# Kernel optimization log

Hardware: AMD Instinct MI355X
Metric: run time of the kernel (lower is better)

Reference implementation:

```python
import jax, jax.numpy as jnp
import numpy as np

NUM_ITERATIONS = 3
EPS = 1e-12


def _squash(s):
    # s: (..., V). squash(s) = |s|^2 * s / ((1+|s|^2) * |s|)
    sq = jnp.sum(s * s, axis=-1, keepdims=True)
    return sq * s / ((1.0 + sq) * jnp.sqrt(sq))


def setup_inputs() -> dict:
    key = jax.random.key(0)
    kx, kw = jax.random.split(key)
    B, L, P, V, Q = 16, 64, 1024, 64, 16
    x = jax.random.normal(kx, (B, P, Q), dtype=jnp.float32)
    W = 0.01 * jax.random.normal(kw, (L, P, V, Q), dtype=jnp.float32)
    return {"x": x, "W": W}


def reference(x, W):
    # u_hat[b,l,p,v] = sum_q W[l,p,v,q] * x[b,p,q]
    u_hat = jnp.einsum('lpvq,bpq->blpv', W, x)  # (B, L, P, V)
    B, L, P, V = u_hat.shape
    b_ij = jnp.zeros((B, L, P), dtype=u_hat.dtype)
    c_ij = None
    v = None
    for it in range(NUM_ITERATIONS):  # small fixed unroll
        c_ij = jax.nn.softmax(b_ij, axis=1)  # softmax over latent caps
        s = jnp.einsum('blp,blpv->blv', c_ij, u_hat)
        v = _squash(s)  # (B, L, V)
        if it < NUM_ITERATIONS - 1:
            # agreement update: b_ij += <v_j, u_hat>
            b_ij = b_ij + jnp.einsum('blv,blpv->blp', v, u_hat)
    # T-score: coupling entropy over latent axis, per primary capsule
    cT = jnp.swapaxes(c_ij, 1, 2)  # (B, P, L)
    entropy = -jnp.sum(cT * jnp.log(cT + EPS), axis=-1)  # (B, P)
    T = jnp.mean(1.0 - entropy / np.log(float(L)))
    # D-score: max over caps of population std (over batch) of activation norms
    v_norm = jnp.linalg.norm(v, axis=-1)  # (B, L)
    D = jnp.max(jnp.std(v_norm, axis=0))
    return v, T, D
```

## Files before the change

kernel.cpp:

```cpp
#include <hip/hip_runtime.h>
#include <hip/hip_bf16.h>

#define B 16
#define L 64
#define P 1024
#define V 64
#define Q 16
#define LN64 4.158883083359672f

#define CHBC 16
#define NCH_BC (P / CHBC)

typedef unsigned short ushort8_t __attribute__((ext_vector_type(8)));
typedef __attribute__((ext_vector_type(8))) short bf16x8;
typedef __attribute__((ext_vector_type(4))) float f32x4;

static __device__ __forceinline__ float bf2f(ushort u) {
    return __uint_as_float(((unsigned int)u) << 16);
}
static __device__ __forceinline__ ushort f2bf(float f) {
    unsigned int x = __float_as_uint(f);
    unsigned int r = (x + 0x7fffu + ((x >> 16) & 1u)) >> 16;
    return (ushort)r;
}
static __device__ __forceinline__ unsigned pk2(float lo, float hi) {
    return (unsigned)f2bf(lo) | ((unsigned)f2bf(hi) << 16);
}

static __device__ __forceinline__ float wsum64(float v) {
#pragma unroll
    for (int m = 32; m > 0; m >>= 1) v += __shfl_xor(v, m, 64);
    return v;
}
static __device__ __forceinline__ float wmax64(float v) {
#pragma unroll
    for (int m = 32; m > 0; m >>= 1) v = fmaxf(v, __shfl_xor(v, m, 64));
    return v;
}

union FragU { uint4 u; bf16x8 s; };

__global__ __launch_bounds__(256, 3) void k_uhat(const float* __restrict__ Wt,
                                                 const float* __restrict__ x,
                                                 ushort* __restrict__ uhat,
                                                 float* __restrict__ sp0) {
    const int t = threadIdx.x;
    const int w = t >> 6;
    const int lane = t & 63;
    const int kb = lane >> 4;
    const int cc = lane & 15;
    const int ch = blockIdx.x;
    const int l = blockIdx.y;
    const int p0 = ch * 32;

    __shared__ unsigned int xstage[32][32][4];

#pragma unroll
    for (int i = 0; i < 16; ++i) {
        const int e = i * 256 + t;
        const int pp = e >> 7, ln = (e >> 2) & 31, m = e & 3;
        const int b = ln & 15, qb = (ln >> 4) * 8;
        const float2 xv = *reinterpret_cast<const float2*>(
            x + ((size_t)b * P + p0 + pp) * Q + qb + 2 * m);
        xstage[pp][ln][m] = pk2(xv.x, xv.y);
    }
    __syncthreads();

    uint4 afe[4], afo[4];
#pragma unroll
    for (int i = 0; i < 4; ++i) {
        if (lane < 32)
            afe[i] = *reinterpret_cast<const uint4*>(&xstage[w * 8 + 2 * i][lane][0]);
        else
            afe[i] = (uint4){0u, 0u, 0u, 0u};
        if (lane >= 32)
            afo[i] = *reinterpret_cast<const uint4*>(&xstage[w * 8 + 2 * i + 1][lane - 32][0]);
        else
            afo[i] = (uint4){0u, 0u, 0u, 0u};
    }

    const float* gW = Wt + ((size_t)l * P + p0 + w * 8) * (V * Q);
    const float* lb = gW + (size_t)(kb >> 1) * (V * Q) + cc * Q + (kb & 1) * 8;

    f32x4 cacc0 = {0.f, 0.f, 0.f, 0.f}, cacc1 = {0.f, 0.f, 0.f, 0.f};
    f32x4 cacc2 = {0.f, 0.f, 0.f, 0.f}, cacc3 = {0.f, 0.f, 0.f, 0.f};
    float4 wl[2][8];

#define LOADP(i_, s_)                                                         \
    {                                                                         \
        const float* bp_ = lb + (size_t)(2 * (i_)) * (V * Q);                 \
        _Pragma("unroll")                                                     \
        for (int g_ = 0; g_ < 4; ++g_) {                                      \
            wl[s_][2 * g_ + 0] = *(const float4*)(bp_ + g_ * 256);            \
            wl[s_][2 * g_ + 1] = *(const float4*)(bp_ + g_ * 256 + 4);        \
        }                                                                     \
    }

#define ONEG(g_, s_, cacc_, ue_, uo_)                                         \
    {                                                                         \
        FragU wf_;                                                            \
        const float4 f0_ = wl[s_][2 * g_ + 0];                                \
        const float4 f1_ = wl[s_][2 * g_ + 1];                                \
        wf_.u = (uint4){pk2(f0_.x, f0_.y), pk2(f0_.z, f0_.w),                 \
                        pk2(f1_.x, f1_.y), pk2(f1_.z, f1_.w)};                \
        f32x4 De_ = __builtin_amdgcn_mfma_f32_16x16x32_bf16(wf_.s, axe_.s,    \
                                                            cacc_, 0, 0, 0);  \
        ue_ = De_ - cacc_;                                                    \
        f32x4 Do_ = __builtin_amdgcn_mfma_f32_16x16x32_bf16(wf_.s, axo_.s,    \
                                                            De_, 0, 0, 0);    \
        uo_ = Do_ - De_;                                                      \
        cacc_ = Do_;                                                          \
    }

#define STOREU(u0_, u1_, u2_, u3_, p_)                                        \
    {                                                                         \
        uint4 A_, Bv_;                                                        \
        A_.x = pk2(u0_[0], u1_[0]); A_.y = pk2(u2_[0], u3_[0]);               \
        A_.z = pk2(u0_[1], u1_[1]); A_.w = pk2(u2_[1], u3_[1]);               \
        Bv_.x = pk2(u0_[2], u1_[2]); Bv_.y = pk2(u2_[2], u3_[2]);             \
        Bv_.z = pk2(u0_[3], u1_[3]); Bv_.w = pk2(u2_[3], u3_[3]);             \
        ushort* ub_ = uhat + (((size_t)l * P + (p_)) * B + cc) * V + kb * 16; \
        *reinterpret_cast<uint4*>(ub_) = A_;                                  \
        *reinterpret_cast<uint4*>(ub_ + 8) = Bv_;                             \
    }

#define COMPUTEP(i_, s_)                                                      \
    {                                                                         \
        FragU axe_; axe_.u = afe[i_];                                         \
        FragU axo_; axo_.u = afo[i_];                                         \
        f32x4 ue0_, ue1_, ue2_, ue3_, uo0_, uo1_, uo2_, uo3_;                 \
        ONEG(0, s_, cacc0, ue0_, uo0_);                                       \
        ONEG(1, s_, cacc1, ue1_, uo1_);                                       \
        ONEG(2, s_, cacc2, ue2_, uo2_);                                       \
        ONEG(3, s_, cacc3, ue3_, uo3_);                                       \
        const int pe_ = p0 + w * 8 + 2 * (i_);                                \
        STOREU(ue0_, ue1_, ue2_, ue3_, pe_);                                  \
        STOREU(uo0_, uo1_, uo2_, uo3_, pe_ + 1);                              \
    }

#define WAITV(N)                                                              \
    asm volatile("s_waitcnt vmcnt(" #N ")" ::: "memory");                     \
    __builtin_amdgcn_sched_barrier(0);

    LOADP(0, 0);
    LOADP(1, 1);
    WAITV(8);  COMPUTEP(0, 0); LOADP(2, 0);
    WAITV(12); COMPUTEP(1, 1); LOADP(3, 1);
    WAITV(12); COMPUTEP(2, 0);
    WAITV(4);  COMPUTEP(3, 1);

    {
        float* sb = sp0 + (((size_t)l * 128 + ch * 4 + w) * 16 + cc) * 64 + kb * 16;
        float4 q0 = {cacc0[0], cacc1[0], cacc2[0], cacc3[0]};
        float4 q1 = {cacc0[1], cacc1[1], cacc2[1], cacc3[1]};
        float4 q2 = {cacc0[2], cacc1[2], cacc2[2], cacc3[2]};
        float4 q3 = {cacc0[3], cacc1[3], cacc2[3], cacc3[3]};
        *reinterpret_cast<float4*>(sb + 0) = q0;
        *reinterpret_cast<float4*>(sb + 4) = q1;
        *reinterpret_cast<float4*>(sb + 8) = q2;
        *reinterpret_cast<float4*>(sb + 12) = q3;
    }
#undef LOADP
#undef ONEG
#undef STOREU
#undef COMPUTEP
#undef WAITV
}

__global__ __launch_bounds__(256) void k_v(const float* __restrict__ sp,
                                           size_t cb, size_t cl, size_t cs,
                                           int nch, float scale, int unperm,
                                           float* __restrict__ vout,
                                           float* __restrict__ norms) {
    const int b = blockIdx.y;
    const int w = threadIdx.x >> 6, lane = threadIdx.x & 63;
    const int l = blockIdx.x * 4 + w;
    const float* p = sp + cb * b + cl * l + lane;
    float s = 0.f;
#pragma unroll 8
    for (int ch = 0; ch < nch; ++ch) s += p[(size_t)ch * cs];
    s *= scale;
    float sq = wsum64(s * s);
    float f = sqrtf(sq) / (1.0f + sq);
    const int vi = unperm ? ((lane & 3) * 16 + (lane >> 4) * 4 + ((lane >> 2) & 3))
                          : lane;
    vout[((size_t)b * L + l) * V + vi] = s * f;
    if (norms && lane == 0) norms[b * L + l] = sq / (1.0f + sq);
}

__global__ __launch_bounds__(512, 4) void k_bc(const ushort* __restrict__ uhat,
                                               const float* __restrict__ vv,
                                               float* __restrict__ bbuf,
                                               float* __restrict__ sp,
                                               float* __restrict__ Tsum,
                                               int add_prev, int do_T) {
    const int ch = blockIdx.x, b = blockIdx.y;
    const int p0 = ch * CHBC;
    const int t = threadIdx.x;
    const int w = t >> 6, lane = t & 63;
    const int pl8 = lane >> 3;
    const int vg8 = lane & 7;
    const int l0 = w * 8;

    __shared__ float vsh[L][V];
    __shared__ float bl[CHBC][L + 1];
    __shared__ float twv[8];

    {
        const float4* vvp = reinterpret_cast<const float4*>(vv + (size_t)b * L * V);
        float4* vshp = reinterpret_cast<float4*>(&vsh[0][0]);
#pragma unroll
        for (int i = 0; i < 2; ++i) vshp[t + i * 512] = vvp[t + i * 512];
    }

    const size_t LSTR = (size_t)P * B * V;
    ushort8_t ur[8][2];
    {
        const ushort* ubase = uhat + (((size_t)l0 * P + p0 + pl8) * B + b) * V + vg8 * 8;
#pragma unroll
        for (int li = 0; li < 8; ++li) {
#pragma unroll
            for (int ph = 0; ph < 2; ++ph)
                ur[li][ph] = *reinterpret_cast<const ushort8_t*>(
                    ubase + (size_t)li * LSTR + (size_t)ph * 8 * B * V);
        }
    }
    __syncthreads();

#pragma unroll
    for (int li = 0; li < 8; ++li) {
        const int l = l0 + li;
        const float4 va = *reinterpret_cast<const float4*>(&vsh[l][vg8 * 8]);
        const float4 vb = *reinterpret_cast<const float4*>(&vsh[l][vg8 * 8 + 4]);
#pragma unroll
        for (int ph = 0; ph < 2; ++ph) {
            float d;
            d = bf2f(ur[li][ph][0]) * va.x;
            d = fmaf(bf2f(ur[li][ph][1]), va.y, d);
            d = fmaf(bf2f(ur[li][ph][2]), va.z, d);
            d = fmaf(bf2f(ur[li][ph][3]), va.w, d);
            d = fmaf(bf2f(ur[li][ph][4]), vb.x, d);
            d = fmaf(bf2f(ur[li][ph][5]), vb.y, d);
            d = fmaf(bf2f(ur[li][ph][6]), vb.z, d);
            d = fmaf(bf2f(ur[li][ph][7]), vb.w, d);
            d += __shfl_xor(d, 1, 64);
            d += __shfl_xor(d, 2, 64);
            d += __shfl_xor(d, 4, 64);
            if (vg8 == 0) bl[ph * 8 + pl8][l] = d;
        }
    }
    __syncthreads();

    float tloc = 0.f;
#pragma unroll
    for (int pi = 0; pi < 2; ++pi) {
        const int pli = w * 2 + pi;
        const int p = p0 + pli;
        float bv = bl[pli][lane];
        float* bp = bbuf + ((size_t)b * P + p) * L;
        if (add_prev) bv += bp[lane];
        bp[lane] = bv;
        float m = wmax64(bv);
        float e = __expf(bv - m);
        float ssum = wsum64(e);
        float cc = e / ssum;
        bl[pli][lane] = cc;
        if (do_T) tloc += cc * __logf(64.0f * (cc + 1e-12f));
    }
    if (do_T) {
        float dsum = wsum64(tloc);
        if (lane == 0) twv[w] = dsum;
    }
    __syncthreads();
    if (do_T && t == 0) {
        float s8 = twv[0] + twv[1] + twv[2] + twv[3] +
                   twv[4] + twv[5] + twv[6] + twv[7];
        atomicAdd(Tsum, s8 * (1.0f / LN64));
    }

    float* spb = sp + (size_t)(b * NCH_BC + ch) * L * V;
#pragma unroll
    for (int li = 0; li < 8; ++li) {
        const int l = l0 + li;
        const float cA = bl[pl8][l];
        const float cB = bl[8 + pl8][l];
        float4 pa, pb;
        pa.x = cA * bf2f(ur[li][0][0]) + cB * bf2f(ur[li][1][0]);
        pa.y = cA * bf2f(ur[li][0][1]) + cB * bf2f(ur[li][1][1]);
        pa.z = cA * bf2f(ur[li][0][2]) + cB * bf2f(ur[li][1][2]);
        pa.w = cA * bf2f(ur[li][0][3]) + cB * bf2f(ur[li][1][3]);
        pb.x = cA * bf2f(ur[li][0][4]) + cB * bf2f(ur[li][1][4]);
        pb.y = cA * bf2f(ur[li][0][5]) + cB * bf2f(ur[li][1][5]);
        pb.z = cA * bf2f(ur[li][0][6]) + cB * bf2f(ur[li][1][6]);
        pb.w = cA * bf2f(ur[li][0][7]) + cB * bf2f(ur[li][1][7]);
#pragma unroll
        for (int m = 8; m <= 32; m <<= 1) {
            pa.x += __shfl_xor(pa.x, m, 64);
            pa.y += __shfl_xor(pa.y, m, 64);
            pa.z += __shfl_xor(pa.z, m, 64);
            pa.w += __shfl_xor(pa.w, m, 64);
            pb.x += __shfl_xor(pb.x, m, 64);
            pb.y += __shfl_xor(pb.y, m, 64);
            pb.z += __shfl_xor(pb.z, m, 64);
            pb.w += __shfl_xor(pb.w, m, 64);
        }
        if (pl8 == 0) {
            *reinterpret_cast<float4*>(spb + (size_t)l * V + vg8 * 8) = pa;
            *reinterpret_cast<float4*>(spb + (size_t)l * V + vg8 * 8 + 4) = pb;
        }
    }
}

__global__ void k_final(const float* __restrict__ Tsum,
                        const float* __restrict__ norms,
                        float* __restrict__ out) {
    const int lane = threadIdx.x & 63;
    float n[B];
    float sum = 0.f;
#pragma unroll
    for (int b = 0; b < B; ++b) { n[b] = norms[b * L + lane]; sum += n[b]; }
    const float mean = sum * (1.0f / B);
    float var = 0.f;
#pragma unroll
    for (int b = 0; b < B; ++b) { float d = n[b] - mean; var = fmaf(d, d, var); }
    var *= (1.0f / B);
    float sd = sqrtf(var);
    float D = wmax64(sd);
    if (lane == 0) {
        out[B * L * V] = Tsum[0] * (1.0f / (B * P));
        out[B * L * V + 1] = D;
    }
}

extern "C" void kernel_launch(void* const* d_in, const int* in_sizes, int n_in,
                              void* d_out, int out_size, void* d_ws, size_t ws_size,
                              hipStream_t stream) {
    const float* x = (const float*)d_in[0];
    const float* W = (const float*)d_in[1];
    float* out = (float*)d_out;

    char* ws = (char*)d_ws;
    ushort* uhat = (ushort*)ws;
    size_t off = (size_t)B * L * P * V * 2;
    float* spbuf = (float*)(ws + off);
    off += (size_t)64 * 128 * 16 * 64 * 4;
    float* vbuf  = (float*)(ws + off); off += (size_t)B * L * V * 4;
    float* bbuf  = (float*)(ws + off); off += (size_t)B * P * L * 4;
    float* norms = (float*)(ws + off); off += (size_t)B * L * 4;
    float* Tsum  = (float*)(ws + off); off += 256;

    hipMemsetAsync(Tsum, 0, sizeof(float), stream);

    hipLaunchKernelGGL(k_uhat, dim3(32, 64), dim3(256), 0, stream, W, x, uhat, spbuf);
    hipLaunchKernelGGL(k_v, dim3(L / 4, B), dim3(256), 0, stream,
                       spbuf, (size_t)64, (size_t)131072, (size_t)1024, 128,
                       1.0f / 64.0f, 0, vbuf, (float*)nullptr);
    hipLaunchKernelGGL(k_bc, dim3(NCH_BC, B), dim3(512), 0, stream,
                       uhat, vbuf, bbuf, spbuf, Tsum, 0, 0);
    hipLaunchKernelGGL(k_v, dim3(L / 4, B), dim3(256), 0, stream,
                       spbuf, (size_t)NCH_BC * L * V, (size_t)V, (size_t)L * V,
                       NCH_BC, 1.0f, 0, vbuf, (float*)nullptr);
    hipLaunchKernelGGL(k_bc, dim3(NCH_BC, B), dim3(512), 0, stream,
                       uhat, vbuf, bbuf, spbuf, Tsum, 1, 1);
    hipLaunchKernelGGL(k_v, dim3(L / 4, B), dim3(256), 0, stream,
                       spbuf, (size_t)NCH_BC * L * V, (size_t)V, (size_t)L * V,
                       NCH_BC, 1.0f, 1, out, norms);
    hipLaunchKernelGGL(k_final, dim3(1), dim3(64), 0, stream, Tsum, norms, out);
}
```

Before: 222.4 us.

## Halve k_uhat tile to 16 capsules per block and reduce partials in LDS

Each k_uhat block now covers 16 primary capsules instead of 32, so the grid doubles to 64x64 blocks. The four waves' partial sums for the first routing iteration are combined in shared memory before being written, which halves the partial-sum buffer and the number of chunks the first k_v pass reads. The hand-scheduled load/compute pipeline with explicit vmcnt waits is replaced by a simple two-step load-then-compute, so loads no longer overlap compute within a block. The intent is more blocks for latency hiding and less partial-sum traffic, at the cost of an extra LDS reduction with a barrier.

```diff
diff --git a/kernel.cpp b/kernel.cpp
--- a/kernel.cpp
+++ b/kernel.cpp
@@ -51,12 +51,13 @@
     const int cc = lane & 15;
     const int ch = blockIdx.x;
     const int l = blockIdx.y;
-    const int p0 = ch * 32;
-
-    __shared__ unsigned int xstage[32][32][4];
-
-#pragma unroll
-    for (int i = 0; i < 16; ++i) {
+    const int p0 = ch * 16;
+
+    __shared__ unsigned int xstage[16][32][4];
+    __shared__ float wred[4][16][64];
+
+#pragma unroll
+    for (int i = 0; i < 8; ++i) {
         const int e = i * 256 + t;
         const int pp = e >> 7, ln = (e >> 2) & 31, m = e & 3;
         const int b = ln & 15, qb = (ln >> 4) * 8;
@@ -66,41 +67,41 @@
     }
     __syncthreads();
 
-    uint4 afe[4], afo[4];
-#pragma unroll
-    for (int i = 0; i < 4; ++i) {
+    uint4 afe[2], afo[2];
+#pragma unroll
+    for (int i = 0; i < 2; ++i) {
         if (lane < 32)
-            afe[i] = *reinterpret_cast<const uint4*>(&xstage[w * 8 + 2 * i][lane][0]);
+            afe[i] = *reinterpret_cast<const uint4*>(&xstage[w * 4 + 2 * i][lane][0]);
         else
             afe[i] = (uint4){0u, 0u, 0u, 0u};
         if (lane >= 32)
-            afo[i] = *reinterpret_cast<const uint4*>(&xstage[w * 8 + 2 * i + 1][lane - 32][0]);
+            afo[i] = *reinterpret_cast<const uint4*>(&xstage[w * 4 + 2 * i + 1][lane - 32][0]);
         else
             afo[i] = (uint4){0u, 0u, 0u, 0u};
     }
 
-    const float* gW = Wt + ((size_t)l * P + p0 + w * 8) * (V * Q);
+    const float* gW = Wt + ((size_t)l * P + p0 + w * 4) * (V * Q);
     const float* lb = gW + (size_t)(kb >> 1) * (V * Q) + cc * Q + (kb & 1) * 8;
 
     f32x4 cacc0 = {0.f, 0.f, 0.f, 0.f}, cacc1 = {0.f, 0.f, 0.f, 0.f};
     f32x4 cacc2 = {0.f, 0.f, 0.f, 0.f}, cacc3 = {0.f, 0.f, 0.f, 0.f};
     float4 wl[2][8];
 
-#define LOADP(i_, s_)                                                         \
-    {                                                                         \
-        const float* bp_ = lb + (size_t)(2 * (i_)) * (V * Q);                 \
-        _Pragma("unroll")                                                     \
-        for (int g_ = 0; g_ < 4; ++g_) {                                      \
-            wl[s_][2 * g_ + 0] = *(const float4*)(bp_ + g_ * 256);            \
-            wl[s_][2 * g_ + 1] = *(const float4*)(bp_ + g_ * 256 + 4);        \
-        }                                                                     \
-    }
-
-#define ONEG(g_, s_, cacc_, ue_, uo_)                                         \
+#pragma unroll
+    for (int i = 0; i < 2; ++i) {
+        const float* bp = lb + (size_t)(2 * i) * (V * Q);
+#pragma unroll
+        for (int g = 0; g < 4; ++g) {
+            wl[i][2 * g + 0] = *(const float4*)(bp + g * 256);
+            wl[i][2 * g + 1] = *(const float4*)(bp + g * 256 + 4);
+        }
+    }
+
+#define ONEG(g_, i_, cacc_, ue_, uo_)                                         \
     {                                                                         \
         FragU wf_;                                                            \
-        const float4 f0_ = wl[s_][2 * g_ + 0];                                \
-        const float4 f1_ = wl[s_][2 * g_ + 1];                                \
+        const float4 f0_ = wl[i_][2 * g_ + 0];                                \
+        const float4 f1_ = wl[i_][2 * g_ + 1];                                \
         wf_.u = (uint4){pk2(f0_.x, f0_.y), pk2(f0_.z, f0_.w),                 \
                         pk2(f1_.x, f1_.y), pk2(f1_.z, f1_.w)};                \
         f32x4 De_ = __builtin_amdgcn_mfma_f32_16x16x32_bf16(wf_.s, axe_.s,    \
@@ -124,47 +125,49 @@
         *reinterpret_cast<uint4*>(ub_ + 8) = Bv_;                             \
     }
 
-#define COMPUTEP(i_, s_)                                                      \
-    {                                                                         \
-        FragU axe_; axe_.u = afe[i_];                                         \
-        FragU axo_; axo_.u = afo[i_];                                         \
-        f32x4 ue0_, ue1_, ue2_, ue3_, uo0_, uo1_, uo2_, uo3_;                 \
-        ONEG(0, s_, cacc0, ue0_, uo0_);                                       \
-        ONEG(1, s_, cacc1, ue1_, uo1_);                                       \
-        ONEG(2, s_, cacc2, ue2_, uo2_);                                       \
-        ONEG(3, s_, cacc3, ue3_, uo3_);                                       \
-        const int pe_ = p0 + w * 8 + 2 * (i_);                                \
-        STOREU(ue0_, ue1_, ue2_, ue3_, pe_);                                  \
-        STOREU(uo0_, uo1_, uo2_, uo3_, pe_ + 1);                              \
-    }
-
-#define WAITV(N)                                                              \
-    asm volatile("s_waitcnt vmcnt(" #N ")" ::: "memory");                     \
-    __builtin_amdgcn_sched_barrier(0);
-
-    LOADP(0, 0);
-    LOADP(1, 1);
-    WAITV(8);  COMPUTEP(0, 0); LOADP(2, 0);
-    WAITV(12); COMPUTEP(1, 1); LOADP(3, 1);
-    WAITV(12); COMPUTEP(2, 0);
-    WAITV(4);  COMPUTEP(3, 1);
+#pragma unroll
+    for (int i = 0; i < 2; ++i) {
+        FragU axe_; axe_.u = afe[i];
+        FragU axo_; axo_.u = afo[i];
+        f32x4 ue0, ue1, ue2, ue3, uo0, uo1, uo2, uo3;
+        ONEG(0, i, cacc0, ue0, uo0);
+        ONEG(1, i, cacc1, ue1, uo1);
+        ONEG(2, i, cacc2, ue2, uo2);
+        ONEG(3, i, cacc3, ue3, uo3);
+        const int pe = p0 + w * 4 + 2 * i;
+        STOREU(ue0, ue1, ue2, ue3, pe);
+        STOREU(uo0, uo1, uo2, uo3, pe + 1);
+    }
+#undef ONEG
+#undef STOREU
 
     {
-        float* sb = sp0 + (((size_t)l * 128 + ch * 4 + w) * 16 + cc) * 64 + kb * 16;
+        float* wb = &wred[w][cc][kb * 16];
         float4 q0 = {cacc0[0], cacc1[0], cacc2[0], cacc3[0]};
         float4 q1 = {cacc0[1], cacc1[1], cacc2[1], cacc3[1]};
         float4 q2 = {cacc0[2], cacc1[2], cacc2[2], cacc3[2]};
         float4 q3 = {cacc0[3], cacc1[3], cacc2[3], cacc3[3]};
-        *reinterpret_cast<float4*>(sb + 0) = q0;
-        *reinterpret_cast<float4*>(sb + 4) = q1;
-        *reinterpret_cast<float4*>(sb + 8) = q2;
-        *reinterpret_cast<float4*>(sb + 12) = q3;
-    }
-#undef LOADP
-#undef ONEG
-#undef STOREU
-#undef COMPUTEP
-#undef WAITV
+        *reinterpret_cast<float4*>(wb + 0) = q0;
+        *reinterpret_cast<float4*>(wb + 4) = q1;
+        *reinterpret_cast<float4*>(wb + 8) = q2;
+        *reinterpret_cast<float4*>(wb + 12) = q3;
+    }
+    __syncthreads();
+    {
+        const int o = t * 4;
+        const int b = o >> 6, sv = o & 63;
+        const float* r0 = &wred[0][b][sv];
+        const float* r1 = &wred[1][b][sv];
+        const float* r2 = &wred[2][b][sv];
+        const float* r3 = &wred[3][b][sv];
+        float4 s;
+        s.x = r0[0] + r1[0] + r2[0] + r3[0];
+        s.y = r0[1] + r1[1] + r2[1] + r3[1];
+        s.z = r0[2] + r1[2] + r2[2] + r3[2];
+        s.w = r0[3] + r1[3] + r2[3] + r3[3];
+        *reinterpret_cast<float4*>(
+            sp0 + (((size_t)l * 64 + ch) * 16 + b) * 64 + sv) = s;
+    }
 }
 
 __global__ __launch_bounds__(256) void k_v(const float* __restrict__ sp,
@@ -351,9 +354,9 @@
 
     hipMemsetAsync(Tsum, 0, sizeof(float), stream);
 
-    hipLaunchKernelGGL(k_uhat, dim3(32, 64), dim3(256), 0, stream, W, x, uhat, spbuf);
+    hipLaunchKernelGGL(k_uhat, dim3(64, 64), dim3(256), 0, stream, W, x, uhat, spbuf);
     hipLaunchKernelGGL(k_v, dim3(L / 4, B), dim3(256), 0, stream,
-                       spbuf, (size_t)64, (size_t)131072, (size_t)1024, 128,
+                       spbuf, (size_t)64, (size_t)65536, (size_t)1024, 64,
                        1.0f / 64.0f, 0, vbuf, (float*)nullptr);
     hipLaunchKernelGGL(k_bc, dim3(NCH_BC, B), dim3(512), 0, stream,
                        uhat, vbuf, bbuf, spbuf, Tsum, 0, 0);
```

Result: faster. 211.4 us (-4.9%).
